# Kernel optimization log

Measured on AMD Instinct MI355X. Metric: run time of the kernel, lower is better.

## Reference

```python
import jax, jax.numpy as jnp
import numpy as np

NEG_SLOPE = 0.2  # PyG GATConv default leaky_relu slope


def gat_layer(x, src, dst, W, a_src, a_dst, n_nodes, heads, ch):
    # x: [N, in_dim]; W: [in_dim, heads*ch]
    h = (x @ W).reshape(n_nodes, heads, ch)              # [N, H, C]
    e_s = jnp.einsum('nhc,hc->nh', h, a_src)             # [N, H]
    e_d = jnp.einsum('nhc,hc->nh', h, a_dst)             # [N, H]
    e = jax.nn.leaky_relu(e_s[src] + e_d[dst], NEG_SLOPE)  # [E, H]
    # segment softmax over incoming edges of each destination node
    m = jax.lax.stop_gradient(jax.ops.segment_max(e, dst, num_segments=n_nodes))
    w = jnp.exp(e - m[dst])                              # [E, H]
    z = jax.ops.segment_sum(w, dst, num_segments=n_nodes)  # [N, H]
    alpha = w / z[dst]                                   # [E, H]
    msg = h[src] * alpha[:, :, None]                     # [E, H, C]
    out = jax.ops.segment_sum(msg, dst, num_segments=n_nodes)  # [N, H, C]
    return out


def setup_inputs() -> dict:
    key = jax.random.key(0)
    ks = jax.random.split(key, 12)
    N, E, D, H = 50000, 800000, 128, 4
    x = jax.random.normal(ks[0], (N, D), dtype=jnp.float32)
    edge_index = jax.random.randint(ks[1], (2, E), 0, N, dtype=jnp.int64)
    s1 = 1.0 / np.sqrt(D)
    s2 = 1.0 / np.sqrt(D * H)
    W1 = jax.random.normal(ks[2], (D, H * D), dtype=jnp.float32) * s1
    a1_src = jax.random.normal(ks[3], (H, D), dtype=jnp.float32) * s1
    a1_dst = jax.random.normal(ks[4], (H, D), dtype=jnp.float32) * s1
    b1 = jax.random.normal(ks[5], (H * D,), dtype=jnp.float32) * 0.01
    W2 = jax.random.normal(ks[6], (H * D, D), dtype=jnp.float32) * s2
    a2_src = jax.random.normal(ks[7], (1, D), dtype=jnp.float32) * s1
    a2_dst = jax.random.normal(ks[8], (1, D), dtype=jnp.float32) * s1
    b2 = jax.random.normal(ks[9], (D,), dtype=jnp.float32) * 0.01
    fc_w = jax.random.normal(ks[10], (D, 1), dtype=jnp.float32) * s1
    fc_b = jax.random.normal(ks[11], (1,), dtype=jnp.float32) * 0.01
    return {"x": x, "edge_index": edge_index, "W1": W1, "a1_src": a1_src,
            "a1_dst": a1_dst, "b1": b1, "W2": W2, "a2_src": a2_src,
            "a2_dst": a2_dst, "b2": b2, "fc_w": fc_w, "fc_b": fc_b}


def reference(x, edge_index, W1, a1_src, a1_dst, b1, W2, a2_src, a2_dst, b2, fc_w, fc_b):
    N, D = x.shape
    H = a1_src.shape[0]
    # add self-loops (PyG GATConv default add_self_loops=True)
    loop = jnp.arange(N, dtype=edge_index.dtype)
    src = jnp.concatenate([edge_index[0], loop])
    dst = jnp.concatenate([edge_index[1], loop])
    # conv1: heads=4, concat=True -> [N, H*D]
    h1 = gat_layer(x, src, dst, W1, a1_src, a1_dst, N, H, D)
    h1 = jax.nn.relu(h1.reshape(N, H * D) + b1)
    # dropout p=0.2 is identity in eval mode
    # conv2: heads=1 -> [N, D]
    h2 = gat_layer(h1, src, dst, W2, a2_src, a2_dst, N, 1, D)
    h2 = h2.reshape(N, D) + b2
    return h2 @ fc_w + fc_b  # [N, 1]
```

## Files before the change

### kernel.cpp

```cpp
#include <hip/hip_runtime.h>
#include <cstdint>
#include <cstddef>

constexpr int kN   = 50000;
constexpr int kE   = 800000;
constexpr int kEt  = kE + kN;
constexpr float kSlope = 0.2f;
constexpr int kScanB = (kN + 255) / 256;
constexpr int kConvB = (kN * 16 + 255) / 256;
constexpr int kHistB = (kEt + 255) / 256;
constexpr int kQuarB = (kN * 16 + 255) / 256;
constexpr int kHChunks = 64;
constexpr int kChunk   = (kEt + kHChunks - 1) / kHChunks;
constexpr int kHRanges = 4;
constexpr int kRangeN  = kN / kHRanges;
constexpr int kRangeH  = kRangeN / 2;
constexpr int kHalfN   = kN / 2;
constexpr int kRows  = 32;
constexpr int kFB    = (kN + kRows - 1) / kRows;
constexpr int kPitch = 520;

typedef __attribute__((ext_vector_type(8))) short bf8_t;
typedef __attribute__((ext_vector_type(4))) float f4_t;
typedef __attribute__((ext_vector_type(2))) float f2_t;

__device__ __align__(16) unsigned short g_xb[(size_t)kN * 128];
__device__ __align__(16) unsigned short g_w1t[4 * 128 * 128];
__device__ __align__(16) float g_u[3][512];
__device__ __align__(16) float g_es1[kN * 4];
__device__ __align__(16) float g_ed1[kN * 4];
__device__ __align__(16) float2 g_sp[kN];
__device__ float g_ed2[kN];
__device__ float g_c0;
__device__ __align__(16) float g_p1s[4 * 128];
__device__ __align__(16) float g_p1d[4 * 128];
__device__ int g_deg[kN];
__device__ int g_ptr[kN + 1];
__device__ int g_rank[kEt];
__device__ __align__(16) unsigned g_bhist[(size_t)kHChunks * kHalfN];
__device__ __align__(16) unsigned g_bbase[(size_t)kHChunks * kHalfN];
__device__ int g_srcs[kEt];
__device__ int g_bsum[kScanB];

__device__ __forceinline__ float lrelu(float x) { return x > 0.f ? x : kSlope * x; }

__device__ __forceinline__ unsigned short f2bf1(float v) {
  unsigned u = __float_as_uint(v);
  unsigned r = (u + 0x7FFFu + ((u >> 16) & 1u)) >> 16;
  return (unsigned short)r;
}

__global__ __launch_bounds__(256) void k_hist(const int* __restrict__ ei) {
  __shared__ unsigned sh[kRangeH];
  const int b = blockIdx.x, t = threadIdx.x;
  const int chunk = b & (kHChunks - 1);
  const int rr = b >> 6;
  const int lo = rr * kRangeN, hi = lo + kRangeN;
  for (int i = t; i < kRangeH; i += 256) sh[i] = 0u;
  __syncthreads();
  const int beg = chunk * kChunk, end = min(beg + kChunk, kEt);
  for (int e = beg + t; e < end; e += 256) {
    int d = (e < kE) ? ei[kE + e] : e - kE;
    if (d >= lo && d < hi) {
      unsigned inc = (d & 1) ? 0x10000u : 1u;
      unsigned old = atomicAdd(&sh[(d - lo) >> 1], inc);
      g_rank[e] = (d & 1) ? (int)(old >> 16) : (int)(old & 0xFFFFu);
    }
  }
  __syncthreads();
  unsigned* dst = g_bhist + (size_t)chunk * kHalfN + rr * kRangeH;
  for (int i = t; i < kRangeH; i += 256) dst[i] = sh[i];
}

__global__ __launch_bounds__(256) void k_pass2() {
  const int i = blockIdx.x * 256 + threadIdx.x;
  if (i >= kHalfN) return;
  unsigned c0 = 0, c1 = 0;
#pragma unroll 4
  for (int b = 0; b < kHChunks; ++b) {
    unsigned v = g_bhist[(size_t)b * kHalfN + i];
    g_bbase[(size_t)b * kHalfN + i] = c0 | (c1 << 16);
    c0 += v & 0xFFFFu;
    c1 += v >> 16;
  }
  *(int2*)&g_deg[2 * i] = make_int2((int)c0, (int)c1);
}

__global__ __launch_bounds__(256) void k_init(const float* __restrict__ x,
    const float* __restrict__ W1, const float* __restrict__ W2,
    const float* __restrict__ a1s, const float* __restrict__ a1d,
    const float* __restrict__ a2s, const float* __restrict__ a2d,
    const float* __restrict__ b2, const float* __restrict__ fcw,
    const float* __restrict__ fcb) {
  const int b = blockIdx.x, t = threadIdx.x;
  if (b < 256) {
    int gid = b * 256 + t;
    int h = gid >> 14, rem = gid & 16383;
    int c = rem >> 7, j = rem & 127;
    float v = W1[(size_t)c * 512 + h * 128 + j];
    g_w1t[((size_t)h * 128 + j) * 128 + c] = f2bf1(v);
  } else if (b < 260) {
    int gid = (b - 256) * 256 + t;
    int which = gid >> 9, idx = gid & 511;
    int h = idx >> 7, k = idx & 127;
    const float* a = which ? a1d : a1s;
    const float* wrow = W1 + (size_t)k * 512 + h * 128;
    float s = 0.f;
#pragma unroll 8
    for (int c = 0; c < 128; ++c) s += wrow[c] * a[h * 128 + c];
    (which ? g_p1d : g_p1s)[idx] = s;
  } else if (b < 266) {
    int gid = (b - 260) * 256 + t;
    if (gid < 1536) {
      int v = gid >> 9, k = gid & 511;
      const float* vv = v == 0 ? a2s : v == 1 ? a2d : fcw;
      const float* wrow = W2 + (size_t)k * 128;
      float s = 0.f;
#pragma unroll 8
      for (int c = 0; c < 128; ++c) s += wrow[c] * vv[c];
      g_u[v][k] = s;
    }
  } else if (b < 267) {
    if (t < 64) {
      float s = b2[t] * fcw[t] + b2[64 + t] * fcw[64 + t];
#pragma unroll
      for (int off = 32; off > 0; off >>= 1) s += __shfl_down(s, off);
      if (t == 0) g_c0 = s + fcb[0];
    }
  } else {
    int g = (b - 267) * 256 + t;
    if (g < kN * 16) {
      const float* xp = x + (size_t)g * 8;
      float4 f0 = *(const float4*)xp;
      float4 f1 = *(const float4*)(xp + 4);
      unsigned w0 = (unsigned)f2bf1(f0.x) | ((unsigned)f2bf1(f0.y) << 16);
      unsigned w1 = (unsigned)f2bf1(f0.z) | ((unsigned)f2bf1(f0.w) << 16);
      unsigned w2 = (unsigned)f2bf1(f1.x) | ((unsigned)f2bf1(f1.y) << 16);
      unsigned w3 = (unsigned)f2bf1(f1.z) | ((unsigned)f2bf1(f1.w) << 16);
      *(uint4*)(g_xb + (size_t)g * 8) = make_uint4(w0, w1, w2, w3);
    }
  }
}

__device__ __forceinline__ void scores1_body(const float* __restrict__ x,
                                             int bid, int t) {
  const int lane = t & 63;
  const int qt = lane >> 4, ql = lane & 15;
  const int n = ((bid * 256 + t) >> 6) * 4 + qt;
  if (n >= kN) return;
  const float* xp = x + (size_t)n * 128 + ql * 8;
  float4 xa = *(const float4*)xp;
  float4 xb = *(const float4*)(xp + 4);
  float s[4], d[4];
#pragma unroll
  for (int h = 0; h < 4; ++h) {
    const float* ps = g_p1s + h * 128 + ql * 8;
    const float* pd = g_p1d + h * 128 + ql * 8;
    s[h] = xa.x * ps[0] + xa.y * ps[1] + xa.z * ps[2] + xa.w * ps[3]
         + xb.x * ps[4] + xb.y * ps[5] + xb.z * ps[6] + xb.w * ps[7];
    d[h] = xa.x * pd[0] + xa.y * pd[1] + xa.z * pd[2] + xa.w * pd[3]
         + xb.x * pd[4] + xb.y * pd[5] + xb.z * pd[6] + xb.w * pd[7];
  }
#pragma unroll
  for (int off = 1; off < 16; off <<= 1) {
#pragma unroll
    for (int h = 0; h < 4; ++h) {
      s[h] += __shfl_xor(s[h], off);
      d[h] += __shfl_xor(d[h], off);
    }
  }
  if (ql == 0) {
    *(float4*)(g_es1 + (size_t)n * 4) = make_float4(s[0], s[1], s[2], s[3]);
    *(float4*)(g_ed1 + (size_t)n * 4) = make_float4(d[0], d[1], d[2], d[3]);
  }
}

__global__ __launch_bounds__(256) void k_scanA(const float* __restrict__ x) {
  __shared__ int s[256];
  const int b = blockIdx.x, t = threadIdx.x;
  if (b >= kScanB) {
    scores1_body(x, b - kScanB, t);
    return;
  }
  const int i = b * 256 + t;
  int d = (i < kN) ? g_deg[i] : 0;
  s[t] = d;
  __syncthreads();
  for (int off = 1; off < 256; off <<= 1) {
    int v = s[t];
    int u = (t >= off) ? s[t - off] : 0;
    __syncthreads();
    s[t] = v + u;
    __syncthreads();
  }
  if (t == 255) g_bsum[b] = s[255];
  if (i < kN) g_ptr[i] = s[t] - d;
}

__global__ __launch_bounds__(256) void k_scanC() {
  __shared__ int s[256];
  const int b = blockIdx.x, t = threadIdx.x;
  int v = (t < kScanB) ? g_bsum[t] : 0;
  s[t] = v;
  __syncthreads();
  for (int off = 1; off < 256; off <<= 1) {
    int a = s[t];
    int u = (t >= off) ? s[t - off] : 0;
    __syncthreads();
    s[t] = a + u;
    __syncthreads();
  }
  const int boff = (b > 0) ? s[b - 1] : 0;
  __syncthreads();
  const int i = b * 256 + t;
  if (i < kN) g_ptr[i] = g_ptr[i] + boff;
  if (b == 0 && t == 0) g_ptr[kN] = kEt;
}

__global__ __launch_bounds__(256) void k_scatter(const int* __restrict__ ei) {
  int e = blockIdx.x * 256 + threadIdx.x;
  if (e >= kEt) return;
  int s, d;
  if (e < kE) { s = ei[e]; d = ei[kE + e]; } else { s = d = e - kE; }
  const int b = e / kChunk;
  unsigned base = g_bbase[(size_t)b * kHalfN + (d >> 1)];
  base = (d & 1) ? (base >> 16) : (base & 0xFFFFu);
  g_srcs[g_ptr[d] + (int)base + g_rank[e]] = s;
}

__global__ __launch_bounds__(512, 4) void k_fagg(const float* __restrict__ b1) {
  __shared__ unsigned short sm[kRows * kPitch];
  __shared__ float sred[4][kRows][3];
  const int t = threadIdx.x;
  const int lane = t & 63, w = t >> 6;
  const int qt = lane >> 4, ql = lane & 15;
  const int row0 = blockIdx.x * kRows;
  const int lbase = qt * 16;

  {
    const int nn = w * 4 + qt;
    const int n = row0 + nn;
    int beg = 0, end = 0;
    float4 ed = make_float4(0.f, 0.f, 0.f, 0.f);
    if (n < kN) {
      beg = g_ptr[n];
      end = g_ptr[n + 1];
      ed = *(const float4*)(g_ed1 + (size_t)n * 4);
    }
    float z0 = 0.f, z1 = 0.f, z2 = 0.f, z3 = 0.f;
    f2_t acc[4][4] = {};
    for (int base = beg; base < end; base += 16) {
      const int cnt = min(16, end - base);
      int s = 0;
      float w0 = 0.f, w1 = 0.f, w2 = 0.f, w3 = 0.f;
      if (ql < cnt) {
        s = g_srcs[base + ql];
        float4 es = *(const float4*)(g_es1 + (size_t)s * 4);
        w0 = __expf(lrelu(es.x + ed.x));
        w1 = __expf(lrelu(es.y + ed.y));
        w2 = __expf(lrelu(es.z + ed.z));
        w3 = __expf(lrelu(es.w + ed.w));
        z0 += w0; z1 += w1; z2 += w2; z3 += w3;
      }
      auto proc = [&](const uint4& uu, int e) {
        float b0 = __shfl(w0, lbase + e), b1v = __shfl(w1, lbase + e);
        float b2 = __shfl(w2, lbase + e), b3 = __shfl(w3, lbase + e);
        f2_t bb0 = b0, bb1 = b1v, bb2 = b2, bb3 = b3;
        unsigned ws[4] = {uu.x, uu.y, uu.z, uu.w};
#pragma unroll
        for (int d = 0; d < 4; ++d) {
          f2_t fv;
          fv[0] = __uint_as_float(ws[d] << 16);
          fv[1] = __uint_as_float(ws[d] & 0xFFFF0000u);
          acc[0][d] += bb0 * fv;
          acc[1][d] += bb1 * fv;
          acc[2][d] += bb2 * fv;
          acc[3][d] += bb3 * fv;
        }
      };
      int e = 0;
      for (; e + 4 <= cnt; e += 4) {
        int sj0 = __shfl(s, lbase + e);
        int sj1 = __shfl(s, lbase + e + 1);
        int sj2 = __shfl(s, lbase + e + 2);
        int sj3 = __shfl(s, lbase + e + 3);
        uint4 u0 = *(const uint4*)(g_xb + (size_t)sj0 * 128 + ql * 8);
        uint4 u1 = *(const uint4*)(g_xb + (size_t)sj1 * 128 + ql * 8);
        uint4 u2 = *(const uint4*)(g_xb + (size_t)sj2 * 128 + ql * 8);
        uint4 u3 = *(const uint4*)(g_xb + (size_t)sj3 * 128 + ql * 8);
        proc(u0, e);
        proc(u1, e + 1);
        proc(u2, e + 2);
        proc(u3, e + 3);
      }
      for (; e < cnt; ++e) {
        int sj = __shfl(s, lbase + e);
        uint4 uu = *(const uint4*)(g_xb + (size_t)sj * 128 + ql * 8);
        proc(uu, e);
      }
    }
#pragma unroll
    for (int off = 1; off < 16; off <<= 1) {
      z0 += __shfl_xor(z0, off); z1 += __shfl_xor(z1, off);
      z2 += __shfl_xor(z2, off); z3 += __shfl_xor(z3, off);
    }
    const bool valid = end > beg;
    const float izz[4] = {valid ? 1.f / z0 : 0.f, valid ? 1.f / z1 : 0.f,
                          valid ? 1.f / z2 : 0.f, valid ? 1.f / z3 : 0.f};
    const int sb = nn * kPitch + ql * 8;
#pragma unroll
    for (int h = 0; h < 4; ++h) {
      unsigned wd[4];
#pragma unroll
      for (int d = 0; d < 4; ++d) {
        f2_t v = acc[h][d] * izz[h];
        wd[d] = (unsigned)f2bf1(v[0]) | ((unsigned)f2bf1(v[1]) << 16);
      }
      *(uint4*)&sm[sb + h * 128] = make_uint4(wd[0], wd[1], wd[2], wd[3]);
    }
  }
  __syncthreads();

  const int wrow = w >> 2, wcol = w & 3;
  const int qo = qt * 8;
  float part[4][3] = {};
#pragma unroll
  for (int h = 0; h < 4; ++h) {
    f4_t h1acc[2] = {};
#pragma unroll
    for (int ks = 0; ks < 128; ks += 32) {
      bf8_t ah = *(const bf8_t*)&sm[(wrow * 16 + ql) * kPitch + h * 128 + ks + qo];
#pragma unroll
      for (int j = 0; j < 2; ++j) {
        size_t gb = ((size_t)h * 128 + wcol * 32 + j * 16 + ql) * 128 + ks + qo;
        bf8_t bh = *(const bf8_t*)&g_w1t[gb];
        h1acc[j] = __builtin_amdgcn_mfma_f32_16x16x32_bf16(ah, bh, h1acc[j], 0, 0, 0);
      }
    }
#pragma unroll
    for (int j = 0; j < 2; ++j) {
      int col = h * 128 + wcol * 32 + j * 16 + ql;
      float bv = b1[col];
      float u0 = g_u[0][col], u1 = g_u[1][col], u2 = g_u[2][col];
#pragma unroll
      for (int reg = 0; reg < 4; ++reg) {
        float v = fmaxf(h1acc[j][reg] + bv, 0.f);
        part[reg][0] += v * u0;
        part[reg][1] += v * u1;
        part[reg][2] += v * u2;
      }
    }
  }
#pragma unroll
  for (int off = 1; off < 16; off <<= 1)
#pragma unroll
    for (int reg = 0; reg < 4; ++reg)
#pragma unroll
      for (int v = 0; v < 3; ++v)
        part[reg][v] += __shfl_xor(part[reg][v], off);
  if (ql == 0) {
#pragma unroll
    for (int reg = 0; reg < 4; ++reg) {
      int rl = wrow * 16 + qt * 4 + reg;
#pragma unroll
      for (int v = 0; v < 3; ++v) sred[wcol][rl][v] = part[reg][v];
    }
  }
  __syncthreads();
  if (t < 96) {
    int row = t / 3, v = t - row * 3;
    float sv = sred[0][row][v] + sred[1][row][v] + sred[2][row][v] + sred[3][row][v];
    int r = row0 + row;
    if (r < kN) {
      if (v == 0)      g_sp[r].x = sv;
      else if (v == 1) g_ed2[r]  = sv;
      else             g_sp[r].y = sv;
    }
  }
}

__global__ __launch_bounds__(256) void k_agg2s(float* __restrict__ out) {
  const int lane = threadIdx.x & 63;
  const int qt = lane >> 4, ql = lane & 15;
  const int n = ((blockIdx.x * 256 + threadIdx.x) >> 6) * 4 + qt;
  if (n >= kN) return;
  const int beg = g_ptr[n], end = g_ptr[n + 1];
  const float ed = g_ed2[n];
  float zp = 0.f, num = 0.f;
  for (int slot = beg + ql; slot < end; slot += 16) {
    int s = g_srcs[slot];
    float2 sp = g_sp[s];
    float w = __expf(lrelu(sp.x + ed));
    zp += w;
    num += w * sp.y;
  }
#pragma unroll
  for (int off = 1; off < 16; off <<= 1) {
    zp  += __shfl_xor(zp, off);
    num += __shfl_xor(num, off);
  }
  if (ql == 0) out[n] = num / zp + g_c0;
}

extern "C" void kernel_launch(void* const* d_in, const int* in_sizes, int n_in,
                              void* d_out, int out_size, void* d_ws, size_t ws_size,
                              hipStream_t stream) {
  const float* x   = (const float*)d_in[0];
  const int*   ei  = (const int*)d_in[1];
  const float* W1  = (const float*)d_in[2];
  const float* a1s = (const float*)d_in[3];
  const float* a1d = (const float*)d_in[4];
  const float* b1  = (const float*)d_in[5];
  const float* W2  = (const float*)d_in[6];
  const float* a2s = (const float*)d_in[7];
  const float* a2d = (const float*)d_in[8];
  const float* b2  = (const float*)d_in[9];
  const float* fcw = (const float*)d_in[10];
  const float* fcb = (const float*)d_in[11];
  float* out = (float*)d_out;
  (void)d_ws; (void)ws_size; (void)in_sizes; (void)n_in; (void)out_size;

  k_hist<<<kHChunks * kHRanges, 256, 0, stream>>>(ei);
  k_init<<<267 + kConvB, 256, 0, stream>>>(x, W1, W2, a1s, a1d,
                                           a2s, a2d, b2, fcw, fcb);
  k_pass2<<<(kHalfN + 255) / 256, 256, 0, stream>>>();
  k_scanA<<<kScanB + kQuarB, 256, 0, stream>>>(x);
  k_scanC<<<kScanB, 256, 0, stream>>>();
  k_scatter<<<kHistB, 256, 0, stream>>>(ei);

  k_fagg<<<kFB, 512, 0, stream>>>(b1);

  k_agg2s<<<kQuarB, 256, 0, stream>>>(out);
}
```

Baseline: 265.5 us.

## Process nodes in degree-sorted order to balance aggregation work

Builds a stable counting-sort permutation of nodes by in-degree (capped at 255) during the scan and scatter kernels. The fused aggregation and second-layer kernels then visit nodes through this permutation, so that 16-lane groups and blocks handle nodes of similar degree. The aim is to cut divergence and load imbalance from the random degree distribution. In exchange it adds an indirection with scattered writes to g_sp/g_ed2 and loses locality of node-contiguous reads, plus a serial per-bin loop over all blocks in block 0 of scanC.

```diff
diff --git a/kernel.cpp b/kernel.cpp
--- a/kernel.cpp
+++ b/kernel.cpp
@@ -41,6 +41,10 @@
 __device__ __align__(16) unsigned g_bbase[(size_t)kHChunks * kHalfN];
 __device__ int g_srcs[kEt];
 __device__ int g_bsum[kScanB];
+__device__ int g_perm[kN];
+__device__ int g_drank[kN];
+__device__ int g_dhist[kScanB * 256];
+__device__ int g_dbase[kScanB * 256];
 
 __device__ __forceinline__ float lrelu(float x) { return x > 0.f ? x : kSlope * x; }
 
@@ -177,11 +181,13 @@
 
 __global__ __launch_bounds__(256) void k_scanA(const float* __restrict__ x) {
   __shared__ int s[256];
+  __shared__ int dh[256];
   const int b = blockIdx.x, t = threadIdx.x;
   if (b >= kScanB) {
     scores1_body(x, b - kScanB, t);
     return;
   }
+  dh[t] = 0;
   const int i = b * 256 + t;
   int d = (i < kN) ? g_deg[i] : 0;
   s[t] = d;
@@ -194,7 +200,12 @@
     __syncthreads();
   }
   if (t == 255) g_bsum[b] = s[255];
-  if (i < kN) g_ptr[i] = s[t] - d;
+  if (i < kN) {
+    g_ptr[i] = s[t] - d;
+    g_drank[i] = atomicAdd(&dh[min(d, 255)], 1);
+  }
+  __syncthreads();
+  g_dhist[b * 256 + t] = dh[t];
 }
 
 __global__ __launch_bounds__(256) void k_scanC() {
@@ -215,9 +226,40 @@
   const int i = b * 256 + t;
   if (i < kN) g_ptr[i] = g_ptr[i] + boff;
   if (b == 0 && t == 0) g_ptr[kN] = kEt;
+
+  if (b == 0) {
+    __syncthreads();
+    int c = 0;
+#pragma unroll 8
+    for (int bb = 0; bb < kScanB; ++bb) {
+      g_dbase[bb * 256 + t] = c;
+      c += g_dhist[bb * 256 + t];
+    }
+    s[t] = c;
+    __syncthreads();
+    for (int off = 1; off < 256; off <<= 1) {
+      int a = s[t];
+      int u = (t >= off) ? s[t - off] : 0;
+      __syncthreads();
+      s[t] = a + u;
+      __syncthreads();
+    }
+    const int binbase = (t > 0) ? s[t - 1] : 0;
+#pragma unroll 8
+    for (int bb = 0; bb < kScanB; ++bb)
+      g_dbase[bb * 256 + t] += binbase;
+  }
 }
 
 __global__ __launch_bounds__(256) void k_scatter(const int* __restrict__ ei) {
+  if (blockIdx.x >= kHistB) {
+    int i = (blockIdx.x - kHistB) * 256 + threadIdx.x;
+    if (i < kN) {
+      int bin = min(g_deg[i], 255);
+      g_perm[g_dbase[(i >> 8) * 256 + bin] + g_drank[i]] = i;
+    }
+    return;
+  }
   int e = blockIdx.x * 256 + threadIdx.x;
   if (e >= kEt) return;
   int s, d;
@@ -238,11 +280,12 @@
   const int lbase = qt * 16;
 
   {
+    const int pos = row0 + w * 4 + qt;
     const int nn = w * 4 + qt;
-    const int n = row0 + nn;
     int beg = 0, end = 0;
     float4 ed = make_float4(0.f, 0.f, 0.f, 0.f);
-    if (n < kN) {
+    if (pos < kN) {
+      const int n = g_perm[pos];
       beg = g_ptr[n];
       end = g_ptr[n + 1];
       ed = *(const float4*)(g_ed1 + (size_t)n * 4);
@@ -370,8 +413,9 @@
   if (t < 96) {
     int row = t / 3, v = t - row * 3;
     float sv = sred[0][row][v] + sred[1][row][v] + sred[2][row][v] + sred[3][row][v];
-    int r = row0 + row;
-    if (r < kN) {
+    int p = row0 + row;
+    if (p < kN) {
+      int r = g_perm[p];
       if (v == 0)      g_sp[r].x = sv;
       else if (v == 1) g_ed2[r]  = sv;
       else             g_sp[r].y = sv;
@@ -382,8 +426,9 @@
 __global__ __launch_bounds__(256) void k_agg2s(float* __restrict__ out) {
   const int lane = threadIdx.x & 63;
   const int qt = lane >> 4, ql = lane & 15;
-  const int n = ((blockIdx.x * 256 + threadIdx.x) >> 6) * 4 + qt;
-  if (n >= kN) return;
+  const int pos = ((blockIdx.x * 256 + threadIdx.x) >> 6) * 4 + qt;
+  if (pos >= kN) return;
+  const int n = g_perm[pos];
   const int beg = g_ptr[n], end = g_ptr[n + 1];
   const float ed = g_ed2[n];
   float zp = 0.f, num = 0.f;
@@ -426,7 +471,7 @@
   k_pass2<<<(kHalfN + 255) / 256, 256, 0, stream>>>();
   k_scanA<<<kScanB + kQuarB, 256, 0, stream>>>(x);
   k_scanC<<<kScanB, 256, 0, stream>>>();
-  k_scatter<<<kHistB, 256, 0, stream>>>(ei);
+  k_scatter<<<kHistB + kScanB, 256, 0, stream>>>(ei);
 
   k_fagg<<<kFB, 512, 0, stream>>>(b1);
 
```

New measurement: 314.8 us. 18.6% more time.
